# Kernel tuning notes

Measured on AMD Instinct MI355X. Metric: run time of the kernel, lower is better.

Reference implementation:

```python
import jax, jax.numpy as jnp
import numpy as np

DIM = 256
HID = 128


def setup_inputs() -> dict:
    key = jax.random.key(0)
    ks = jax.random.split(key, 10)
    B, T = 8, 2048
    s_in = 1.0 / np.sqrt(DIM)
    s_h = 1.0 / np.sqrt(HID)
    return {
        "x": jax.random.normal(ks[0], (B, T, DIM), jnp.float32),
        "adapt_bias": jax.random.normal(ks[1], (B, T, T), jnp.float32),
        "Wq": jax.random.uniform(ks[2], (HID, DIM), jnp.float32, -s_in, s_in),
        "bq": jax.random.uniform(ks[3], (HID,), jnp.float32, -s_in, s_in),
        "Wk": jax.random.uniform(ks[4], (HID, DIM), jnp.float32, -s_in, s_in),
        "bk": jax.random.uniform(ks[5], (HID,), jnp.float32, -s_in, s_in),
        "Wv": jax.random.uniform(ks[6], (HID, DIM), jnp.float32, -s_in, s_in),
        "bv": jax.random.uniform(ks[7], (HID,), jnp.float32, -s_in, s_in),
        "Wp": jax.random.uniform(ks[8], (DIM, HID), jnp.float32, -s_h, s_h),
        "bp": jax.random.uniform(ks[9], (DIM,), jnp.float32, -s_h, s_h),
    }


def reference(x, adapt_bias, Wq, bq, Wk, bk, Wv, bv, Wp, bp):
    # y = x (default). Q,K,V: [B,T,H]
    Q = jnp.einsum('btd,hd->bth', x, Wq) + bq
    K = jnp.einsum('btd,hd->bth', x, Wk) + bk
    V = jnp.einsum('btd,hd->bth', x, Wv) + bv
    Q_sig = jax.nn.sigmoid(Q)
    ab = jax.nn.softmax(adapt_bias, axis=-1)        # [B,T,T]
    Ksm = jax.nn.softmax(K, axis=1)                 # softmax over time dim
    eab = jnp.exp(ab)                               # [B,T,T]
    eK = jnp.exp(Ksm)                               # [B,T,H]
    num = jnp.einsum('bts,bsh->bth', eab, eK * V)
    den = jnp.einsum('bts,bsh->bth', eab, eK)
    Yt = Q_sig * (num / den)                        # [B,T,H]
    return jnp.einsum('bth,dh->btd', Yt, Wp) + bp   # [B,T,DIM]
```

## Files before the change

kernel.cpp:

```cpp
#include <hip/hip_runtime.h>
#include <hip/hip_bf16.h>

#define B_ 8
#define T_ 2048
#define D_ 256
#define H_ 128

typedef float f32x4 __attribute__((ext_vector_type(4)));
typedef short bf16x8 __attribute__((ext_vector_type(8)));
typedef unsigned short u16x8 __attribute__((ext_vector_type(8)));

__device__ __forceinline__ unsigned short f2bf(float f){
  union { float f; unsigned u; } v; v.f = f;
  unsigned u = v.u;
  unsigned r = (u + 0x7FFFu + ((u >> 16) & 1u)) >> 16;
  return (unsigned short)r;
}

__device__ __forceinline__ float bf2f(unsigned short us){
  union { unsigned u; float f; } v; v.u = ((unsigned)us) << 16; return v.f;
}

#define GLL16(g, l) __builtin_amdgcn_global_load_lds( \
    (const __attribute__((address_space(1))) void*)(g), \
    (__attribute__((address_space(3))) void*)(l), 16, 0, 0)

__device__ __forceinline__ float blk_reduce(float v, bool is_max, float* sbuf){
  for(int o = 32; o > 0; o >>= 1){
    float t = __shfl_xor(v, o);
    v = is_max ? fmaxf(v, t) : (v + t);
  }
  int w = threadIdx.x >> 6;
  __syncthreads();
  if((threadIdx.x & 63) == 0) sbuf[w] = v;
  __syncthreads();
  float r = sbuf[0];
  for(int i = 1; i < 4; i++) r = is_max ? fmaxf(r, sbuf[i]) : (r + sbuf[i]);
  return r;
}

__global__ __launch_bounds__(256) void qkv_kernel(
    const float* __restrict__ x,
    const float* __restrict__ Wq, const float* __restrict__ bq,
    const float* __restrict__ Wk, const float* __restrict__ bk,
    const float* __restrict__ Wv, const float* __restrict__ bv,
    float* __restrict__ Qsig, unsigned short* __restrict__ Ktb,
    unsigned short* __restrict__ Vtb)
{
  const int mat = blockIdx.y;
  const int g0  = blockIdx.x * 64;
  const int tid = threadIdx.x;
  const float* W   = (mat == 0) ? Wq : (mat == 1) ? Wk : Wv;
  const float* bia = (mat == 0) ? bq : (mat == 1) ? bk : bv;

  __shared__ __align__(16) short As[64 * 32];
  __shared__ __align__(16) short Ws[128 * 32];
  __shared__ float tbuf[64][129];

  const int w = tid >> 6, lane = tid & 63, rl = lane & 15, kg = lane >> 4;
  f32x4 acc[8];
  for(int i = 0; i < 8; i++) acc[i] = (f32x4){0.f, 0.f, 0.f, 0.f};

  const int c = tid & 31, r8 = tid >> 5;
  for(int kk = 0; kk < 256; kk += 32){
    __syncthreads();
    for(int p = 0; p < 8; p++){
      int rr = r8 + p * 8;
      As[rr * 32 + c] = (short)f2bf(x[(size_t)(g0 + rr) * 256 + kk + c]);
    }
    for(int p = 0; p < 16; p++){
      int hh = r8 + p * 8;
      Ws[hh * 32 + c] = (short)f2bf(W[(size_t)hh * 256 + kk + c]);
    }
    __syncthreads();
    bf16x8 a = *(const bf16x8*)&As[(w * 16 + rl) * 32 + kg * 8];
    for(int cf = 0; cf < 8; cf++){
      bf16x8 bb = *(const bf16x8*)&Ws[(cf * 16 + rl) * 32 + kg * 8];
      acc[cf] = __builtin_amdgcn_mfma_f32_16x16x32_bf16(a, bb, acc[cf], 0, 0, 0);
    }
  }

  const int b = g0 >> 11, t0 = g0 & 2047;
  if(mat == 0){
    for(int cf = 0; cf < 8; cf++){
      int h = cf * 16 + rl;
      float bh = bia[h];
      for(int r = 0; r < 4; r++){
        int tl = w * 16 + kg * 4 + r;
        float v = acc[cf][r] + bh;
        Qsig[(size_t)(g0 + tl) * 128 + h] = 1.f / (1.f + __expf(-v));
      }
    }
  } else {
    for(int cf = 0; cf < 8; cf++){
      int h = cf * 16 + rl;
      float bh = bia[h];
      for(int r = 0; r < 4; r++){
        int tl = w * 16 + kg * 4 + r;
        tbuf[tl][h] = acc[cf][r] + bh;
      }
    }
    __syncthreads();
    unsigned short* dst = (mat == 1) ? Ktb : Vtb;
    int h = tid >> 1, part = tid & 1;
    unsigned short* drow = dst + (size_t)(b * 128 + h) * 2048 + t0 + part * 32;
#pragma unroll
    for(int i = 0; i < 32; i += 8){
      u16x8 o;
#pragma unroll
      for(int j = 0; j < 8; j++) o[j] = f2bf(tbuf[part * 32 + i + j][h]);
      *(u16x8*)(drow + i) = o;
    }
  }
}

__global__ __launch_bounds__(256) void colsm_kernel(
    const unsigned short* __restrict__ Ktb, const unsigned short* __restrict__ Vtb,
    unsigned short* __restrict__ Mt)
{
  __shared__ float sbuf[4];
  const int b  = blockIdx.x >> 5;
  const int hg = blockIdx.x & 31;
  const int tid = threadIdx.x;
  for(int i = 0; i < 4; i++){
    int h = hg * 4 + i;
    const unsigned short* kr = Ktb + (size_t)(b * 128 + h) * 2048;
    const unsigned short* vr = Vtb + (size_t)(b * 128 + h) * 2048;
    u16x8 k8 = *(const u16x8*)(kr + tid * 8);
    u16x8 v8 = *(const u16x8*)(vr + tid * 8);
    float kf[8];
#pragma unroll
    for(int j = 0; j < 8; j++) kf[j] = bf2f(k8[j]);
    float m = kf[0];
#pragma unroll
    for(int j = 1; j < 8; j++) m = fmaxf(m, kf[j]);
    m = blk_reduce(m, true, sbuf);
    float s = 0.f;
#pragma unroll
    for(int j = 0; j < 8; j++) s += __expf(kf[j] - m);
    s = blk_reduce(s, false, sbuf);
    float iz = 1.f / s;
    u16x8 pv, pe;
#pragma unroll
    for(int j = 0; j < 8; j++){
      float e = __expf(__expf(kf[j] - m) * iz);
      pv[j] = f2bf(e * bf2f(v8[j]));
      pe[j] = f2bf(e);
    }
    *(u16x8*)(Mt + (size_t)(b * 256 + h) * 2048 + tid * 8) = pv;
    *(u16x8*)(Mt + (size_t)(b * 256 + 128 + h) * 2048 + tid * 8) = pe;
  }
}

__global__ __launch_bounds__(256) void softexp_kernel(
    const float* __restrict__ ab, unsigned short* __restrict__ eab)
{
  __shared__ float sbuf[4];
  const size_t row = blockIdx.x;
  const float* r = ab + row * 2048;
  const int tid = threadIdx.x;
  float4 v0 = *(const float4*)(r + tid * 4);
  float4 v1 = *(const float4*)(r + tid * 4 + 1024);
  float m = fmaxf(fmaxf(fmaxf(v0.x, v0.y), fmaxf(v0.z, v0.w)),
                  fmaxf(fmaxf(v1.x, v1.y), fmaxf(v1.z, v1.w)));
  m = blk_reduce(m, true, sbuf);
  float e0x = __expf(v0.x - m), e0y = __expf(v0.y - m);
  float e0z = __expf(v0.z - m), e0w = __expf(v0.w - m);
  float e1x = __expf(v1.x - m), e1y = __expf(v1.y - m);
  float e1z = __expf(v1.z - m), e1w = __expf(v1.w - m);
  float s = e0x + e0y + e0z + e0w + e1x + e1y + e1z + e1w;
  s = blk_reduce(s, false, sbuf);
  float iz = 1.f / s;
  ushort4 o;
  o.x = f2bf(__expf(e0x * iz)); o.y = f2bf(__expf(e0y * iz));
  o.z = f2bf(__expf(e0z * iz)); o.w = f2bf(__expf(e0w * iz));
  *(ushort4*)(eab + row * 2048 + tid * 4) = o;
  o.x = f2bf(__expf(e1x * iz)); o.y = f2bf(__expf(e1y * iz));
  o.z = f2bf(__expf(e1z * iz)); o.w = f2bf(__expf(e1w * iz));
  *(ushort4*)(eab + row * 2048 + tid * 4 + 1024) = o;
}

__global__ __launch_bounds__(256) void aft_gemm6(
    const unsigned short* __restrict__ eab,
    const unsigned short* __restrict__ Mt,
    const float* __restrict__ Qsig,
    unsigned short* __restrict__ Yt)
{
  __shared__ __align__(16) unsigned short As2[3][64 * 64];
  __shared__ __align__(16) unsigned short Bs2[3][128 * 64];

  const int bid = blockIdx.x;
  const int b   = bid & 7;
  const int idx = bid >> 3;
  const int rt  = idx >> 1;
  const int hb  = idx & 1;
  const int t0  = rt * 64;
  const int h0  = hb * 64;

  const int tid = threadIdx.x;
  const int w = tid >> 6, lane = tid & 63;
  const int rl = lane & 15, kg = lane >> 4;
  const int wr = w >> 1, wc = w & 1;

  const int lr = lane >> 3;
  const int cc = (lane & 7) ^ lr;

  const size_t rowbase = (size_t)b * 2048 + t0;
  const unsigned short* a_src = eab + (rowbase + (size_t)(w * 16 + lr)) * 2048 + cc * 8;
  const int mtrow = (w < 2) ? (h0 + w * 32 + lr) : (128 + h0 + (w - 2) * 32 + lr);
  const unsigned short* b_src = Mt + ((size_t)b * 256 + mtrow) * 2048 + cc * 8;

  f32x4 acc[2][4];
#pragma unroll
  for(int i = 0; i < 2; i++)
#pragma unroll
    for(int j = 0; j < 4; j++) acc[i][j] = (f32x4){0.f, 0.f, 0.f, 0.f};

  auto stage = [&](int buf, int t){
#pragma unroll
    for(int i = 0; i < 2; i++)
      GLL16(a_src + (size_t)i * 8 * 2048 + t * 64, &As2[buf][(w * 16 + i * 8) * 64]);
#pragma unroll
    for(int i = 0; i < 4; i++)
      GLL16(b_src + (size_t)i * 8 * 2048 + t * 64, &Bs2[buf][(w * 32 + i * 8) * 64]);
  };

  const int rx = rl & 7;
  stage(0, 0);
  stage(1, 1);

  int cur = 0;
  for(int t = 0; t < 32; ++t){
    if(t < 31) asm volatile("s_waitcnt vmcnt(6)" ::: "memory");
    else       asm volatile("s_waitcnt vmcnt(0)" ::: "memory");
    __builtin_amdgcn_s_barrier();
    if(t < 30){
      int nb = cur + 2; if(nb >= 3) nb -= 3;
      stage(nb, t + 2);
    }
    __builtin_amdgcn_s_setprio(1);
#pragma unroll
    for(int ks = 0; ks < 2; ++ks){
      const int slot = ((ks * 4 + kg) ^ rx) * 8;
      bf16x8 a0 = *(const bf16x8*)&As2[cur][(wr * 32 + rl) * 64 + slot];
      bf16x8 a1 = *(const bf16x8*)&As2[cur][(wr * 32 + 16 + rl) * 64 + slot];
#pragma unroll
      for(int cf = 0; cf < 4; ++cf){
        const int brow = ((cf < 2) ? (wc * 32 + cf * 16)
                                   : (64 + wc * 32 + (cf - 2) * 16)) + rl;
        bf16x8 bb = *(const bf16x8*)&Bs2[cur][brow * 64 + slot];
        acc[0][cf] = __builtin_amdgcn_mfma_f32_16x16x32_bf16(a0, bb, acc[0][cf], 0, 0, 0);
        acc[1][cf] = __builtin_amdgcn_mfma_f32_16x16x32_bf16(a1, bb, acc[1][cf], 0, 0, 0);
      }
    }
    __builtin_amdgcn_s_setprio(0);
    asm volatile("s_waitcnt lgkmcnt(0)" ::: "memory");
    __builtin_amdgcn_sched_barrier(0);
    cur += 1; if(cur >= 3) cur -= 3;
  }

#pragma unroll
  for(int rf = 0; rf < 2; ++rf)
#pragma unroll
    for(int cf = 0; cf < 2; ++cf){
      const int h = h0 + wc * 32 + cf * 16 + rl;
#pragma unroll
      for(int r = 0; r < 4; ++r){
        const int tl = wr * 32 + rf * 16 + kg * 4 + r;
        const size_t g = rowbase + tl;
        float num = acc[rf][cf][r], den = acc[rf][cf + 2][r];
        float q = Qsig[g * 128 + h];
        Yt[g * 128 + h] = f2bf(q * num / den);
      }
    }
}

__global__ __launch_bounds__(256) void outproj_kernel(
    const unsigned short* __restrict__ Yt, const float* __restrict__ Wp,
    const float* __restrict__ bp, float* __restrict__ out)
{
  __shared__ __align__(16) short As[64 * 32];
  __shared__ __align__(16) short Bs[256 * 32];
  const int g0 = blockIdx.x * 64;
  const int tid = threadIdx.x;
  const int w = tid >> 6, lane = tid & 63, rl = lane & 15, kg = lane >> 4;
  f32x4 acc[16];
  for(int i = 0; i < 16; i++) acc[i] = (f32x4){0.f, 0.f, 0.f, 0.f};

  const int ar = tid >> 2, apart = tid & 3;
  const int c = tid & 31, dr = tid >> 5;
  for(int k = 0; k < 128; k += 32){
    __syncthreads();
    *(uint4*)&As[ar * 32 + apart * 8] =
        *(const uint4*)(Yt + (size_t)(g0 + ar) * 128 + k + apart * 8);
    for(int p = 0; p < 32; p++){
      int d = dr + p * 8;
      Bs[d * 32 + c] = (short)f2bf(Wp[(size_t)d * 128 + k + c]);
    }
    __syncthreads();
    bf16x8 a = *(const bf16x8*)&As[(w * 16 + rl) * 32 + kg * 8];
    for(int cf = 0; cf < 16; cf++){
      bf16x8 bb = *(const bf16x8*)&Bs[(cf * 16 + rl) * 32 + kg * 8];
      acc[cf] = __builtin_amdgcn_mfma_f32_16x16x32_bf16(a, bb, acc[cf], 0, 0, 0);
    }
  }
  for(int cf = 0; cf < 16; cf++){
    int d = cf * 16 + rl;
    float bpd = bp[d];
    for(int r = 0; r < 4; r++){
      int tl = w * 16 + kg * 4 + r;
      out[(size_t)(g0 + tl) * 256 + d] = acc[cf][r] + bpd;
    }
  }
}

extern "C" void kernel_launch(void* const* d_in, const int* in_sizes, int n_in,
                              void* d_out, int out_size, void* d_ws, size_t ws_size,
                              hipStream_t stream)
{
  const float* x  = (const float*)d_in[0];
  const float* ab = (const float*)d_in[1];
  const float* Wq = (const float*)d_in[2];
  const float* bq = (const float*)d_in[3];
  const float* Wk = (const float*)d_in[4];
  const float* bk = (const float*)d_in[5];
  const float* Wv = (const float*)d_in[6];
  const float* bv = (const float*)d_in[7];
  const float* Wp = (const float*)d_in[8];
  const float* bp = (const float*)d_in[9];
  float* out = (float*)d_out;

  char* ws = (char*)d_ws;
  float* Qsig          = (float*)(ws);
  unsigned short* Ktb  = (unsigned short*)(ws + 8388608);
  unsigned short* Vtb  = (unsigned short*)(ws + 12582912);
  unsigned short* Mt   = (unsigned short*)(ws + 16777216);
  unsigned short* eab  = (unsigned short*)(ws + 25165824);
  unsigned short* Yt   = (unsigned short*)(ws + 8388608);

  qkv_kernel<<<dim3(256, 3), 256, 0, stream>>>(x, Wq, bq, Wk, bk, Wv, bv, Qsig, Ktb, Vtb);
  colsm_kernel<<<256, 256, 0, stream>>>(Ktb, Vtb, Mt);
  softexp_kernel<<<16384, 256, 0, stream>>>(ab, eab);
  aft_gemm6<<<512, 256, 0, stream>>>(eab, Mt, Qsig, Yt);
  outproj_kernel<<<256, 256, 0, stream>>>(Yt, Wp, bp, out);
}
```

Before: 97.45 us.

## Merge softmax-exp into QKV launch and load GEMM A operand directly to registers

Merges the adapt_bias softmax-exp kernel and the QKV projection into one launch, with the block index selecting the role, so the two independent phases can overlap and one launch is dropped. In the AFT GEMM, the A operand (eab) is no longer staged through LDS. Each lane loads its fragments straight from global memory into double-buffered registers one iteration ahead, while B keeps the three-stage LDS pipeline. This cuts LDS traffic and footprint, but the fused kernel now carries the larger QKV shared-memory allocation for every softmax block, which may lower occupancy. The direct A loads are also less coalesced.

Result: slower. 113.6 us (+16.5%).

```diff
diff --git a/kernel.cpp b/kernel.cpp
--- a/kernel.cpp
+++ b/kernel.cpp
@@ -39,7 +39,8 @@
   return r;
 }
 
-__global__ __launch_bounds__(256) void qkv_kernel(
+__global__ __launch_bounds__(256) void fused1_kernel(
+    const float* __restrict__ ab, unsigned short* __restrict__ eab,
     const float* __restrict__ x,
     const float* __restrict__ Wq, const float* __restrict__ bq,
     const float* __restrict__ Wk, const float* __restrict__ bk,
@@ -47,15 +48,43 @@
     float* __restrict__ Qsig, unsigned short* __restrict__ Ktb,
     unsigned short* __restrict__ Vtb)
 {
-  const int mat = blockIdx.y;
-  const int g0  = blockIdx.x * 64;
-  const int tid = threadIdx.x;
-  const float* W   = (mat == 0) ? Wq : (mat == 1) ? Wk : Wv;
-  const float* bia = (mat == 0) ? bq : (mat == 1) ? bk : bv;
-
   __shared__ __align__(16) short As[64 * 32];
   __shared__ __align__(16) short Ws[128 * 32];
   __shared__ float tbuf[64][129];
+  __shared__ float sbuf[4];
+
+  const int tid = threadIdx.x;
+
+  if(blockIdx.x < 16384){
+    const size_t row = blockIdx.x;
+    const float* r = ab + row * 2048;
+    float4 v0 = *(const float4*)(r + tid * 4);
+    float4 v1 = *(const float4*)(r + tid * 4 + 1024);
+    float m = fmaxf(fmaxf(fmaxf(v0.x, v0.y), fmaxf(v0.z, v0.w)),
+                    fmaxf(fmaxf(v1.x, v1.y), fmaxf(v1.z, v1.w)));
+    m = blk_reduce(m, true, sbuf);
+    float e0x = __expf(v0.x - m), e0y = __expf(v0.y - m);
+    float e0z = __expf(v0.z - m), e0w = __expf(v0.w - m);
+    float e1x = __expf(v1.x - m), e1y = __expf(v1.y - m);
+    float e1z = __expf(v1.z - m), e1w = __expf(v1.w - m);
+    float s = e0x + e0y + e0z + e0w + e1x + e1y + e1z + e1w;
+    s = blk_reduce(s, false, sbuf);
+    float iz = 1.f / s;
+    ushort4 o;
+    o.x = f2bf(__expf(e0x * iz)); o.y = f2bf(__expf(e0y * iz));
+    o.z = f2bf(__expf(e0z * iz)); o.w = f2bf(__expf(e0w * iz));
+    *(ushort4*)(eab + row * 2048 + tid * 4) = o;
+    o.x = f2bf(__expf(e1x * iz)); o.y = f2bf(__expf(e1y * iz));
+    o.z = f2bf(__expf(e1z * iz)); o.w = f2bf(__expf(e1w * iz));
+    *(ushort4*)(eab + row * 2048 + tid * 4 + 1024) = o;
+    return;
+  }
+
+  const int rb  = blockIdx.x - 16384;
+  const int mat = rb >> 8;
+  const int g0  = (rb & 255) * 64;
+  const float* W   = (mat == 0) ? Wq : (mat == 1) ? Wk : Wv;
+  const float* bia = (mat == 0) ? bq : (mat == 1) ? bk : bv;
 
   const int w = tid >> 6, lane = tid & 63, rl = lane & 15, kg = lane >> 4;
   f32x4 acc[8];
@@ -152,41 +181,12 @@
   }
 }
 
-__global__ __launch_bounds__(256) void softexp_kernel(
-    const float* __restrict__ ab, unsigned short* __restrict__ eab)
-{
-  __shared__ float sbuf[4];
-  const size_t row = blockIdx.x;
-  const float* r = ab + row * 2048;
-  const int tid = threadIdx.x;
-  float4 v0 = *(const float4*)(r + tid * 4);
-  float4 v1 = *(const float4*)(r + tid * 4 + 1024);
-  float m = fmaxf(fmaxf(fmaxf(v0.x, v0.y), fmaxf(v0.z, v0.w)),
-                  fmaxf(fmaxf(v1.x, v1.y), fmaxf(v1.z, v1.w)));
-  m = blk_reduce(m, true, sbuf);
-  float e0x = __expf(v0.x - m), e0y = __expf(v0.y - m);
-  float e0z = __expf(v0.z - m), e0w = __expf(v0.w - m);
-  float e1x = __expf(v1.x - m), e1y = __expf(v1.y - m);
-  float e1z = __expf(v1.z - m), e1w = __expf(v1.w - m);
-  float s = e0x + e0y + e0z + e0w + e1x + e1y + e1z + e1w;
-  s = blk_reduce(s, false, sbuf);
-  float iz = 1.f / s;
-  ushort4 o;
-  o.x = f2bf(__expf(e0x * iz)); o.y = f2bf(__expf(e0y * iz));
-  o.z = f2bf(__expf(e0z * iz)); o.w = f2bf(__expf(e0w * iz));
-  *(ushort4*)(eab + row * 2048 + tid * 4) = o;
-  o.x = f2bf(__expf(e1x * iz)); o.y = f2bf(__expf(e1y * iz));
-  o.z = f2bf(__expf(e1z * iz)); o.w = f2bf(__expf(e1w * iz));
-  *(ushort4*)(eab + row * 2048 + tid * 4 + 1024) = o;
-}
-
-__global__ __launch_bounds__(256) void aft_gemm6(
+__global__ __launch_bounds__(256) void aft_gemm7(
     const unsigned short* __restrict__ eab,
     const unsigned short* __restrict__ Mt,
     const float* __restrict__ Qsig,
     unsigned short* __restrict__ Yt)
 {
-  __shared__ __align__(16) unsigned short As2[3][64 * 64];
   __shared__ __align__(16) unsigned short Bs2[3][128 * 64];
 
   const int bid = blockIdx.x;
@@ -206,58 +206,70 @@
   const int cc = (lane & 7) ^ lr;
 
   const size_t rowbase = (size_t)b * 2048 + t0;
-  const unsigned short* a_src = eab + (rowbase + (size_t)(w * 16 + lr)) * 2048 + cc * 8;
   const int mtrow = (w < 2) ? (h0 + w * 32 + lr) : (128 + h0 + (w - 2) * 32 + lr);
   const unsigned short* b_src = Mt + ((size_t)b * 256 + mtrow) * 2048 + cc * 8;
 
+  const unsigned short* a_lane = eab + (rowbase + (size_t)(wr * 32 + rl)) * 2048 + kg * 8;
+
   f32x4 acc[2][4];
 #pragma unroll
   for(int i = 0; i < 2; i++)
 #pragma unroll
     for(int j = 0; j < 4; j++) acc[i][j] = (f32x4){0.f, 0.f, 0.f, 0.f};
 
-  auto stage = [&](int buf, int t){
-#pragma unroll
-    for(int i = 0; i < 2; i++)
-      GLL16(a_src + (size_t)i * 8 * 2048 + t * 64, &As2[buf][(w * 16 + i * 8) * 64]);
+  auto stageB = [&](int buf, int t){
 #pragma unroll
     for(int i = 0; i < 4; i++)
       GLL16(b_src + (size_t)i * 8 * 2048 + t * 64, &Bs2[buf][(w * 32 + i * 8) * 64]);
   };
 
+  #define LOADA(bank, t) do { \
+    bank[0][0] = *(const bf16x8*)(a_lane + (t) * 64); \
+    bank[0][1] = *(const bf16x8*)(a_lane + (t) * 64 + 32); \
+    bank[1][0] = *(const bf16x8*)(a_lane + 16 * 2048 + (t) * 64); \
+    bank[1][1] = *(const bf16x8*)(a_lane + 16 * 2048 + (t) * 64 + 32); \
+  } while(0)
+
   const int rx = rl & 7;
-  stage(0, 0);
-  stage(1, 1);
+
+  #define BODY(t, curA, nextA) do { \
+    if((t) < 31) asm volatile("s_waitcnt vmcnt(4)" ::: "memory"); \
+    else         asm volatile("s_waitcnt vmcnt(0)" ::: "memory"); \
+    __builtin_amdgcn_s_barrier(); \
+    if((t) < 30){ int nb = cur + 2; if(nb >= 3) nb -= 3; stageB(nb, (t) + 2); } \
+    if((t) < 31){ LOADA(nextA, (t) + 1); } \
+    __builtin_amdgcn_s_setprio(1); \
+    _Pragma("unroll") \
+    for(int ks = 0; ks < 2; ++ks){ \
+      const int slot = ((ks * 4 + kg) ^ rx) * 8; \
+      _Pragma("unroll") \
+      for(int cf = 0; cf < 4; ++cf){ \
+        const int brow = ((cf < 2) ? (wc * 32 + cf * 16) \
+                                   : (64 + wc * 32 + (cf - 2) * 16)) + rl; \
+        bf16x8 bb = *(const bf16x8*)&Bs2[cur][brow * 64 + slot]; \
+        acc[0][cf] = __builtin_amdgcn_mfma_f32_16x16x32_bf16(curA[0][ks], bb, acc[0][cf], 0, 0, 0); \
+        acc[1][cf] = __builtin_amdgcn_mfma_f32_16x16x32_bf16(curA[1][ks], bb, acc[1][cf], 0, 0, 0); \
+      } \
+    } \
+    __builtin_amdgcn_s_setprio(0); \
+    asm volatile("s_waitcnt lgkmcnt(0)" ::: "memory"); \
+    __builtin_amdgcn_sched_barrier(0); \
+    cur += 1; if(cur >= 3) cur -= 3; \
+  } while(0)
+
+  bf16x8 A0[2][2], A1[2][2];
+  LOADA(A0, 0);
+  stageB(0, 0);
+  stageB(1, 1);
 
   int cur = 0;
-  for(int t = 0; t < 32; ++t){
-    if(t < 31) asm volatile("s_waitcnt vmcnt(6)" ::: "memory");
-    else       asm volatile("s_waitcnt vmcnt(0)" ::: "memory");
-    __builtin_amdgcn_s_barrier();
-    if(t < 30){
-      int nb = cur + 2; if(nb >= 3) nb -= 3;
-      stage(nb, t + 2);
-    }
-    __builtin_amdgcn_s_setprio(1);
-#pragma unroll
-    for(int ks = 0; ks < 2; ++ks){
-      const int slot = ((ks * 4 + kg) ^ rx) * 8;
-      bf16x8 a0 = *(const bf16x8*)&As2[cur][(wr * 32 + rl) * 64 + slot];
-      bf16x8 a1 = *(const bf16x8*)&As2[cur][(wr * 32 + 16 + rl) * 64 + slot];
-#pragma unroll
-      for(int cf = 0; cf < 4; ++cf){
-        const int brow = ((cf < 2) ? (wc * 32 + cf * 16)
-                                   : (64 + wc * 32 + (cf - 2) * 16)) + rl;
-        bf16x8 bb = *(const bf16x8*)&Bs2[cur][brow * 64 + slot];
-        acc[0][cf] = __builtin_amdgcn_mfma_f32_16x16x32_bf16(a0, bb, acc[0][cf], 0, 0, 0);
-        acc[1][cf] = __builtin_amdgcn_mfma_f32_16x16x32_bf16(a1, bb, acc[1][cf], 0, 0, 0);
-      }
-    }
-    __builtin_amdgcn_s_setprio(0);
-    asm volatile("s_waitcnt lgkmcnt(0)" ::: "memory");
-    __builtin_amdgcn_sched_barrier(0);
-    cur += 1; if(cur >= 3) cur -= 3;
-  }
+#pragma unroll 1
+  for(int t = 0; t < 32; t += 2){
+    BODY(t,     A0, A1);
+    BODY(t + 1, A1, A0);
+  }
+  #undef BODY
+  #undef LOADA
 
 #pragma unroll
   for(int rf = 0; rf < 2; ++rf)
@@ -338,9 +350,9 @@
   unsigned short* eab  = (unsigned short*)(ws + 25165824);
   unsigned short* Yt   = (unsigned short*)(ws + 8388608);
 
-  qkv_kernel<<<dim3(256, 3), 256, 0, stream>>>(x, Wq, bq, Wk, bk, Wv, bv, Qsig, Ktb, Vtb);
+  fused1_kernel<<<17152, 256, 0, stream>>>(ab, eab, x, Wq, bq, Wk, bk, Wv, bv,
+                                           Qsig, Ktb, Vtb);
   colsm_kernel<<<256, 256, 0, stream>>>(Ktb, Vtb, Mt);
-  softexp_kernel<<<16384, 256, 0, stream>>>(ab, eab);
-  aft_gemm6<<<512, 256, 0, stream>>>(eab, Mt, Qsig, Yt);
+  aft_gemm7<<<512, 256, 0, stream>>>(eab, Mt, Qsig, Yt);
   outproj_kernel<<<256, 256, 0, stream>>>(Yt, Wp, bp, out);
 }
```

## Fuse QKV projections per block, store Qsig as bf16, double-buffer AFT GEMM

Applied to the files above, without the earlier changes.

The QKV projection now computes all three matrices in one block over 32 rows, so each tile of x is loaded and converted once instead of three times. Sigmoid(Q) is stored in bf16 to halve its write and read traffic. The main AFT GEMM moves from a triple-buffered LDS pipeline to a double-buffered one: fragments are loaded into registers, then a barrier runs before the next stage is issued, which lowers LDS use but adds a second barrier per iteration. The bf16 Qsig adds some rounding error to the output.

Result: slower. 176.9 us (+81.5%).

```diff
diff --git a/kernel.cpp b/kernel.cpp
--- a/kernel.cpp
+++ b/kernel.cpp
@@ -39,76 +39,94 @@
   return r;
 }
 
-__global__ __launch_bounds__(256) void qkv_kernel(
+__global__ __launch_bounds__(256) void qkv3_kernel(
     const float* __restrict__ x,
     const float* __restrict__ Wq, const float* __restrict__ bq,
     const float* __restrict__ Wk, const float* __restrict__ bk,
     const float* __restrict__ Wv, const float* __restrict__ bv,
-    float* __restrict__ Qsig, unsigned short* __restrict__ Ktb,
+    unsigned short* __restrict__ Qsigb, unsigned short* __restrict__ Ktb,
     unsigned short* __restrict__ Vtb)
 {
-  const int mat = blockIdx.y;
-  const int g0  = blockIdx.x * 64;
-  const int tid = threadIdx.x;
-  const float* W   = (mat == 0) ? Wq : (mat == 1) ? Wk : Wv;
-  const float* bia = (mat == 0) ? bq : (mat == 1) ? bk : bv;
-
-  __shared__ __align__(16) short As[64 * 32];
-  __shared__ __align__(16) short Ws[128 * 32];
-  __shared__ float tbuf[64][129];
-
+  __shared__ __align__(16) short As[32 * 32];
+  __shared__ __align__(16) short Ws[3][128 * 32];
+  __shared__ float tbuf[32][129];
+
+  const int g0  = blockIdx.x * 32;
+  const int tid = threadIdx.x;
   const int w = tid >> 6, lane = tid & 63, rl = lane & 15, kg = lane >> 4;
-  f32x4 acc[8];
-  for(int i = 0; i < 8; i++) acc[i] = (f32x4){0.f, 0.f, 0.f, 0.f};
+  const int wr = w >> 1, wc = w & 1;
+
+  const float* Wm[3] = {Wq, Wk, Wv};
+
+  f32x4 acc[3][4];
+#pragma unroll
+  for(int m = 0; m < 3; m++)
+#pragma unroll
+    for(int j = 0; j < 4; j++) acc[m][j] = (f32x4){0.f, 0.f, 0.f, 0.f};
 
   const int c = tid & 31, r8 = tid >> 5;
   for(int kk = 0; kk < 256; kk += 32){
     __syncthreads();
-    for(int p = 0; p < 8; p++){
+#pragma unroll
+    for(int p = 0; p < 4; p++){
       int rr = r8 + p * 8;
       As[rr * 32 + c] = (short)f2bf(x[(size_t)(g0 + rr) * 256 + kk + c]);
     }
-    for(int p = 0; p < 16; p++){
-      int hh = r8 + p * 8;
-      Ws[hh * 32 + c] = (short)f2bf(W[(size_t)hh * 256 + kk + c]);
-    }
-    __syncthreads();
-    bf16x8 a = *(const bf16x8*)&As[(w * 16 + rl) * 32 + kg * 8];
-    for(int cf = 0; cf < 8; cf++){
-      bf16x8 bb = *(const bf16x8*)&Ws[(cf * 16 + rl) * 32 + kg * 8];
-      acc[cf] = __builtin_amdgcn_mfma_f32_16x16x32_bf16(a, bb, acc[cf], 0, 0, 0);
-    }
+#pragma unroll
+    for(int m = 0; m < 3; m++)
+#pragma unroll
+      for(int p = 0; p < 16; p++){
+        int hh = r8 + p * 8;
+        Ws[m][hh * 32 + c] = (short)f2bf(Wm[m][(size_t)hh * 256 + kk + c]);
+      }
+    __syncthreads();
+    bf16x8 a = *(const bf16x8*)&As[(wr * 16 + rl) * 32 + kg * 8];
+#pragma unroll
+    for(int m = 0; m < 3; m++)
+#pragma unroll
+      for(int cf = 0; cf < 4; cf++){
+        bf16x8 bb = *(const bf16x8*)&Ws[m][(wc * 64 + cf * 16 + rl) * 32 + kg * 8];
+        acc[m][cf] = __builtin_amdgcn_mfma_f32_16x16x32_bf16(a, bb, acc[m][cf], 0, 0, 0);
+      }
   }
 
   const int b = g0 >> 11, t0 = g0 & 2047;
-  if(mat == 0){
-    for(int cf = 0; cf < 8; cf++){
-      int h = cf * 16 + rl;
+
+#pragma unroll
+  for(int cf = 0; cf < 4; cf++){
+    int h = wc * 64 + cf * 16 + rl;
+    float bh = bq[h];
+#pragma unroll
+    for(int r = 0; r < 4; r++){
+      int tl = wr * 16 + kg * 4 + r;
+      float v = acc[0][cf][r] + bh;
+      Qsigb[(size_t)(g0 + tl) * 128 + h] = f2bf(1.f / (1.f + __expf(-v)));
+    }
+  }
+
+#pragma unroll
+  for(int m = 1; m < 3; m++){
+    const float* bia = (m == 1) ? bk : bv;
+    __syncthreads();
+#pragma unroll
+    for(int cf = 0; cf < 4; cf++){
+      int h = wc * 64 + cf * 16 + rl;
       float bh = bia[h];
+#pragma unroll
       for(int r = 0; r < 4; r++){
-        int tl = w * 16 + kg * 4 + r;
-        float v = acc[cf][r] + bh;
-        Qsig[(size_t)(g0 + tl) * 128 + h] = 1.f / (1.f + __expf(-v));
-      }
-    }
-  } else {
-    for(int cf = 0; cf < 8; cf++){
-      int h = cf * 16 + rl;
-      float bh = bia[h];
-      for(int r = 0; r < 4; r++){
-        int tl = w * 16 + kg * 4 + r;
-        tbuf[tl][h] = acc[cf][r] + bh;
-      }
-    }
-    __syncthreads();
-    unsigned short* dst = (mat == 1) ? Ktb : Vtb;
+        int tl = wr * 16 + kg * 4 + r;
+        tbuf[tl][h] = acc[m][cf][r] + bh;
+      }
+    }
+    __syncthreads();
+    unsigned short* dst = (m == 1) ? Ktb : Vtb;
     int h = tid >> 1, part = tid & 1;
-    unsigned short* drow = dst + (size_t)(b * 128 + h) * 2048 + t0 + part * 32;
-#pragma unroll
-    for(int i = 0; i < 32; i += 8){
+    unsigned short* drow = dst + (size_t)(b * 128 + h) * 2048 + t0 + part * 16;
+#pragma unroll
+    for(int i = 0; i < 16; i += 8){
       u16x8 o;
 #pragma unroll
-      for(int j = 0; j < 8; j++) o[j] = f2bf(tbuf[part * 32 + i + j][h]);
+      for(int j = 0; j < 8; j++) o[j] = f2bf(tbuf[part * 16 + i + j][h]);
       *(u16x8*)(drow + i) = o;
     }
   }
@@ -180,14 +198,14 @@
   *(ushort4*)(eab + row * 2048 + tid * 4 + 1024) = o;
 }
 
-__global__ __launch_bounds__(256) void aft_gemm6(
+__global__ __launch_bounds__(256) void aft_gemm4(
     const unsigned short* __restrict__ eab,
     const unsigned short* __restrict__ Mt,
-    const float* __restrict__ Qsig,
+    const unsigned short* __restrict__ Qsigb,
     unsigned short* __restrict__ Yt)
 {
-  __shared__ __align__(16) unsigned short As2[3][64 * 64];
-  __shared__ __align__(16) unsigned short Bs2[3][128 * 64];
+  __shared__ __align__(16) unsigned short As2[2][64 * 64];
+  __shared__ __align__(16) unsigned short Bs2[2][128 * 64];
 
   const int bid = blockIdx.x;
   const int b   = bid & 7;
@@ -229,34 +247,42 @@
   stage(0, 0);
   stage(1, 1);
 
-  int cur = 0;
   for(int t = 0; t < 32; ++t){
+    const int cur = t & 1;
     if(t < 31) asm volatile("s_waitcnt vmcnt(6)" ::: "memory");
     else       asm volatile("s_waitcnt vmcnt(0)" ::: "memory");
     __builtin_amdgcn_s_barrier();
-    if(t < 30){
-      int nb = cur + 2; if(nb >= 3) nb -= 3;
-      stage(nb, t + 2);
-    }
-    __builtin_amdgcn_s_setprio(1);
+    asm volatile("" ::: "memory");
+
+    bf16x8 af[2][2], bfr[2][4];
 #pragma unroll
     for(int ks = 0; ks < 2; ++ks){
       const int slot = ((ks * 4 + kg) ^ rx) * 8;
-      bf16x8 a0 = *(const bf16x8*)&As2[cur][(wr * 32 + rl) * 64 + slot];
-      bf16x8 a1 = *(const bf16x8*)&As2[cur][(wr * 32 + 16 + rl) * 64 + slot];
+      af[ks][0] = *(const bf16x8*)&As2[cur][(wr * 32 + rl) * 64 + slot];
+      af[ks][1] = *(const bf16x8*)&As2[cur][(wr * 32 + 16 + rl) * 64 + slot];
 #pragma unroll
       for(int cf = 0; cf < 4; ++cf){
         const int brow = ((cf < 2) ? (wc * 32 + cf * 16)
                                    : (64 + wc * 32 + (cf - 2) * 16)) + rl;
-        bf16x8 bb = *(const bf16x8*)&Bs2[cur][brow * 64 + slot];
-        acc[0][cf] = __builtin_amdgcn_mfma_f32_16x16x32_bf16(a0, bb, acc[0][cf], 0, 0, 0);
-        acc[1][cf] = __builtin_amdgcn_mfma_f32_16x16x32_bf16(a1, bb, acc[1][cf], 0, 0, 0);
-      }
-    }
-    __builtin_amdgcn_s_setprio(0);
+        bfr[ks][cf] = *(const bf16x8*)&Bs2[cur][brow * 64 + slot];
+      }
+    }
     asm volatile("s_waitcnt lgkmcnt(0)" ::: "memory");
     __builtin_amdgcn_sched_barrier(0);
-    cur += 1; if(cur >= 3) cur -= 3;
+    __builtin_amdgcn_s_barrier();
+    asm volatile("" ::: "memory");
+
+    if(t < 30) stage(cur, t + 2);
+
+    __builtin_amdgcn_s_setprio(1);
+#pragma unroll
+    for(int ks = 0; ks < 2; ++ks)
+#pragma unroll
+      for(int cf = 0; cf < 4; ++cf){
+        acc[0][cf] = __builtin_amdgcn_mfma_f32_16x16x32_bf16(af[ks][0], bfr[ks][cf], acc[0][cf], 0, 0, 0);
+        acc[1][cf] = __builtin_amdgcn_mfma_f32_16x16x32_bf16(af[ks][1], bfr[ks][cf], acc[1][cf], 0, 0, 0);
+      }
+    __builtin_amdgcn_s_setprio(0);
   }
 
 #pragma unroll
@@ -269,7 +295,7 @@
         const int tl = wr * 32 + rf * 16 + kg * 4 + r;
         const size_t g = rowbase + tl;
         float num = acc[rf][cf][r], den = acc[rf][cf + 2][r];
-        float q = Qsig[g * 128 + h];
+        float q = bf2f(Qsigb[g * 128 + h]);
         Yt[g * 128 + h] = f2bf(q * num / den);
       }
     }
@@ -331,16 +357,16 @@
   float* out = (float*)d_out;
 
   char* ws = (char*)d_ws;
-  float* Qsig          = (float*)(ws);
-  unsigned short* Ktb  = (unsigned short*)(ws + 8388608);
-  unsigned short* Vtb  = (unsigned short*)(ws + 12582912);
-  unsigned short* Mt   = (unsigned short*)(ws + 16777216);
-  unsigned short* eab  = (unsigned short*)(ws + 25165824);
-  unsigned short* Yt   = (unsigned short*)(ws + 8388608);
-
-  qkv_kernel<<<dim3(256, 3), 256, 0, stream>>>(x, Wq, bq, Wk, bk, Wv, bv, Qsig, Ktb, Vtb);
+  unsigned short* Qsigb = (unsigned short*)(ws);
+  unsigned short* Ktb   = (unsigned short*)(ws + 8388608);
+  unsigned short* Vtb   = (unsigned short*)(ws + 12582912);
+  unsigned short* Mt    = (unsigned short*)(ws + 16777216);
+  unsigned short* eab   = (unsigned short*)(ws + 25165824);
+  unsigned short* Yt    = (unsigned short*)(ws + 8388608);
+
+  qkv3_kernel<<<512, 256, 0, stream>>>(x, Wq, bq, Wk, bk, Wv, bv, Qsigb, Ktb, Vtb);
   colsm_kernel<<<256, 256, 0, stream>>>(Ktb, Vtb, Mt);
   softexp_kernel<<<16384, 256, 0, stream>>>(ab, eab);
-  aft_gemm6<<<512, 256, 0, stream>>>(eab, Mt, Qsig, Yt);
+  aft_gemm4<<<512, 256, 0, stream>>>(eab, Mt, Qsigb, Yt);
   outproj_kernel<<<256, 256, 0, stream>>>(Yt, Wp, bp, out);
 }
```

## Switch AFT GEMM to double-buffered pipeline with fragment prefetch and bf16 Qsig

Applied to the files above, without the earlier changes.

The AFT GEMM kernel goes from a triple-buffered LDS ring to a double buffer. Each iteration now loads every A/B fragment into registers, passes a second barrier, issues the global-to-LDS load for tile t+2 into the freed buffer, and then runs the MFMAs. This cuts shared memory use from about 72KB to 48KB per block, which may allow more resident blocks, at the cost of an extra barrier per iteration and more fragment registers. Separately, the sigmoid(Q) intermediate is stored as bf16 instead of fp32, halving that tensor's write and read traffic with a small precision loss.

Result: faster. 92.94 us (-4.6%).

```diff
diff --git a/kernel.cpp b/kernel.cpp
--- a/kernel.cpp
+++ b/kernel.cpp
@@ -44,7 +44,7 @@
     const float* __restrict__ Wq, const float* __restrict__ bq,
     const float* __restrict__ Wk, const float* __restrict__ bk,
     const float* __restrict__ Wv, const float* __restrict__ bv,
-    float* __restrict__ Qsig, unsigned short* __restrict__ Ktb,
+    unsigned short* __restrict__ Qsigb, unsigned short* __restrict__ Ktb,
     unsigned short* __restrict__ Vtb)
 {
   const int mat = blockIdx.y;
@@ -88,7 +88,7 @@
       for(int r = 0; r < 4; r++){
         int tl = w * 16 + kg * 4 + r;
         float v = acc[cf][r] + bh;
-        Qsig[(size_t)(g0 + tl) * 128 + h] = 1.f / (1.f + __expf(-v));
+        Qsigb[(size_t)(g0 + tl) * 128 + h] = f2bf(1.f / (1.f + __expf(-v)));
       }
     }
   } else {
@@ -180,14 +180,14 @@
   *(ushort4*)(eab + row * 2048 + tid * 4 + 1024) = o;
 }
 
-__global__ __launch_bounds__(256) void aft_gemm6(
+__global__ __launch_bounds__(256) void aft_gemm4(
     const unsigned short* __restrict__ eab,
     const unsigned short* __restrict__ Mt,
-    const float* __restrict__ Qsig,
+    const unsigned short* __restrict__ Qsigb,
     unsigned short* __restrict__ Yt)
 {
-  __shared__ __align__(16) unsigned short As2[3][64 * 64];
-  __shared__ __align__(16) unsigned short Bs2[3][128 * 64];
+  __shared__ __align__(16) unsigned short As2[2][64 * 64];
+  __shared__ __align__(16) unsigned short Bs2[2][128 * 64];
 
   const int bid = blockIdx.x;
   const int b   = bid & 7;
@@ -229,34 +229,42 @@
   stage(0, 0);
   stage(1, 1);
 
-  int cur = 0;
   for(int t = 0; t < 32; ++t){
+    const int cur = t & 1;
     if(t < 31) asm volatile("s_waitcnt vmcnt(6)" ::: "memory");
     else       asm volatile("s_waitcnt vmcnt(0)" ::: "memory");
     __builtin_amdgcn_s_barrier();
-    if(t < 30){
-      int nb = cur + 2; if(nb >= 3) nb -= 3;
-      stage(nb, t + 2);
-    }
-    __builtin_amdgcn_s_setprio(1);
+    asm volatile("" ::: "memory");
+
+    bf16x8 af[2][2], bfr[2][4];
 #pragma unroll
     for(int ks = 0; ks < 2; ++ks){
       const int slot = ((ks * 4 + kg) ^ rx) * 8;
-      bf16x8 a0 = *(const bf16x8*)&As2[cur][(wr * 32 + rl) * 64 + slot];
-      bf16x8 a1 = *(const bf16x8*)&As2[cur][(wr * 32 + 16 + rl) * 64 + slot];
+      af[ks][0] = *(const bf16x8*)&As2[cur][(wr * 32 + rl) * 64 + slot];
+      af[ks][1] = *(const bf16x8*)&As2[cur][(wr * 32 + 16 + rl) * 64 + slot];
 #pragma unroll
       for(int cf = 0; cf < 4; ++cf){
         const int brow = ((cf < 2) ? (wc * 32 + cf * 16)
                                    : (64 + wc * 32 + (cf - 2) * 16)) + rl;
-        bf16x8 bb = *(const bf16x8*)&Bs2[cur][brow * 64 + slot];
-        acc[0][cf] = __builtin_amdgcn_mfma_f32_16x16x32_bf16(a0, bb, acc[0][cf], 0, 0, 0);
-        acc[1][cf] = __builtin_amdgcn_mfma_f32_16x16x32_bf16(a1, bb, acc[1][cf], 0, 0, 0);
-      }
-    }
-    __builtin_amdgcn_s_setprio(0);
+        bfr[ks][cf] = *(const bf16x8*)&Bs2[cur][brow * 64 + slot];
+      }
+    }
     asm volatile("s_waitcnt lgkmcnt(0)" ::: "memory");
     __builtin_amdgcn_sched_barrier(0);
-    cur += 1; if(cur >= 3) cur -= 3;
+    __builtin_amdgcn_s_barrier();
+    asm volatile("" ::: "memory");
+
+    if(t < 30) stage(cur, t + 2);
+
+    __builtin_amdgcn_s_setprio(1);
+#pragma unroll
+    for(int ks = 0; ks < 2; ++ks)
+#pragma unroll
+      for(int cf = 0; cf < 4; ++cf){
+        acc[0][cf] = __builtin_amdgcn_mfma_f32_16x16x32_bf16(af[ks][0], bfr[ks][cf], acc[0][cf], 0, 0, 0);
+        acc[1][cf] = __builtin_amdgcn_mfma_f32_16x16x32_bf16(af[ks][1], bfr[ks][cf], acc[1][cf], 0, 0, 0);
+      }
+    __builtin_amdgcn_s_setprio(0);
   }
 
 #pragma unroll
@@ -269,7 +277,7 @@
         const int tl = wr * 32 + rf * 16 + kg * 4 + r;
         const size_t g = rowbase + tl;
         float num = acc[rf][cf][r], den = acc[rf][cf + 2][r];
-        float q = Qsig[g * 128 + h];
+        float q = bf2f(Qsigb[g * 128 + h]);
         Yt[g * 128 + h] = f2bf(q * num / den);
       }
     }
@@ -331,16 +339,16 @@
   float* out = (float*)d_out;
 
   char* ws = (char*)d_ws;
-  float* Qsig          = (float*)(ws);
-  unsigned short* Ktb  = (unsigned short*)(ws + 8388608);
-  unsigned short* Vtb  = (unsigned short*)(ws + 12582912);
-  unsigned short* Mt   = (unsigned short*)(ws + 16777216);
-  unsigned short* eab  = (unsigned short*)(ws + 25165824);
-  unsigned short* Yt   = (unsigned short*)(ws + 8388608);
-
-  qkv_kernel<<<dim3(256, 3), 256, 0, stream>>>(x, Wq, bq, Wk, bk, Wv, bv, Qsig, Ktb, Vtb);
+  unsigned short* Qsigb = (unsigned short*)(ws);
+  unsigned short* Ktb   = (unsigned short*)(ws + 8388608);
+  unsigned short* Vtb   = (unsigned short*)(ws + 12582912);
+  unsigned short* Mt    = (unsigned short*)(ws + 16777216);
+  unsigned short* eab   = (unsigned short*)(ws + 25165824);
+  unsigned short* Yt    = (unsigned short*)(ws + 8388608);
+
+  qkv_kernel<<<dim3(256, 3), 256, 0, stream>>>(x, Wq, bq, Wk, bk, Wv, bv, Qsigb, Ktb, Vtb);
   colsm_kernel<<<256, 256, 0, stream>>>(Ktb, Vtb, Mt);
   softexp_kernel<<<16384, 256, 0, stream>>>(ab, eab);
-  aft_gemm6<<<512, 256, 0, stream>>>(eab, Mt, Qsig, Yt);
+  aft_gemm4<<<512, 256, 0, stream>>>(eab, Mt, Qsigb, Yt);
   outproj_kernel<<<256, 256, 0, stream>>>(Yt, Wp, bp, out);
 }
```
